# Performance work log

Hardware: AMD Instinct MI355X
Metric: run time of the kernel (lower is better)

The kernel has to match this reference:

```python
import jax, jax.numpy as jnp
import numpy as np

N_NODES = 50000
N_EDGES = 800000
IN_CH = 128
HID_CH = 128


def glorot(key, shape):
    fan_in, fan_out = shape[0], shape[1]
    lim = np.sqrt(6.0 / (fan_in + fan_out)).astype(np.float32)
    return jax.random.uniform(key, shape, jnp.float32, -lim, lim)


def setup_inputs() -> dict:
    key = jax.random.key(0)
    k1, k2, k3, k4 = jax.random.split(key, 4)
    x = jax.random.normal(k1, (N_NODES, IN_CH), jnp.float32)
    edge_index = jax.random.randint(k2, (2, N_EDGES), 0, N_NODES, jnp.int64)
    W1 = glorot(k3, (IN_CH, HID_CH))
    b1 = jnp.zeros((HID_CH,), jnp.float32)
    W2 = glorot(k4, (HID_CH, HID_CH))
    b2 = jnp.zeros((HID_CH,), jnp.float32)
    return {"x": x, "edge_index": edge_index, "W1": W1, "b1": b1, "W2": W2, "b2": b2}


def _gcn_conv(x, W, b, src, dst, n_nodes):
    # PyG GCNConv: h = D^{-1/2} (A + I) D^{-1/2} (x W) + b
    h = x @ W  # [N, H] transform first (as in PyG)
    loops = jnp.arange(n_nodes, dtype=src.dtype)
    s = jnp.concatenate([src, loops])  # add self-loops
    d = jnp.concatenate([dst, loops])
    deg = jnp.zeros((n_nodes,), h.dtype).at[d].add(1.0)
    dinv = jnp.where(deg > 0, jax.lax.rsqrt(deg), 0.0)
    coef = dinv[s] * dinv[d]  # [E+N]
    msg = h[s] * coef[:, None]  # gather + scale
    out = jax.ops.segment_sum(msg, d, num_segments=n_nodes)  # scatter-add
    return out + b


def reference(x, edge_index, W1, b1, W2, b2):
    src, dst = edge_index[0], edge_index[1]
    n = x.shape[0]
    h = jax.nn.relu(_gcn_conv(x, W1, b1, src, dst, n))
    h = jax.nn.relu(_gcn_conv(h, W2, b2, src, dst, n))
    return h
```

## Files before the change

### kernel.cpp

```cpp
#include <hip/hip_runtime.h>

#define N_NODES 50000
#define N_EDGES 800000
#define CH 128
#define NBUCK 196
#define B_BIN 250
#define CHUNK 3200
#define G_GEMM 782

typedef __attribute__((ext_vector_type(8))) short bf16x8;
typedef __attribute__((ext_vector_type(8))) unsigned short u16x8;
typedef __attribute__((ext_vector_type(4))) float f32x4;

__device__ __forceinline__ float bf2f(unsigned short u) {
    union { unsigned int i; float f; } c;
    c.i = ((unsigned int)u) << 16;
    return c.f;
}
__device__ __forceinline__ unsigned short f2bf(float f) {
    union { float f; unsigned int i; } c;
    c.f = f;
    unsigned int lsb = (c.i >> 16) & 1u;
    c.i += 0x7fffu + lsb;
    return (unsigned short)(c.i >> 16);
}

__global__ __launch_bounds__(256) void k_wt(const float* __restrict__ Wa,
                                            const float* __restrict__ Wb,
                                            unsigned short* __restrict__ Wta,
                                            unsigned short* __restrict__ Wtb) {
    const float* W = blockIdx.x ? Wb : Wa;
    unsigned short* Wt = blockIdx.x ? Wtb : Wta;
    const int tid = threadIdx.x;
    for (int i = 0; i < 64; ++i) {
        int idx = i * 256 + tid;
        int n = idx >> 7, kk = idx & 127;
        Wt[idx] = f2bf(W[kk * CH + n]);
    }
}

__global__ __launch_bounds__(256) void k_mega(
        const int* __restrict__ ei, int* __restrict__ blk_base,
        const float* __restrict__ X, const unsigned short* __restrict__ Wt1,
        unsigned short* __restrict__ HS1u) {
    const int tid = threadIdx.x;
    const int b = blockIdx.x;

    if (b < B_BIN) {
        __shared__ int h[NBUCK];
        for (int i = tid; i < NBUCK; i += 256) h[i] = 0;
        __syncthreads();
        const int e0 = b * CHUNK;
        const int* dst = ei + N_EDGES;
        for (int i = tid; i < CHUNK; i += 256)
            atomicAdd(&h[dst[e0 + i] >> 8], 1);
        __syncthreads();
        for (int k = tid; k < NBUCK; k += 256)
            blk_base[b * NBUCK + k] = h[k];
        return;
    }

    const int gb = b - B_BIN;
    const int l = tid & 63, w = tid >> 6;
    const int lm = l & 15, lk = l >> 4;
    const int row0 = gb * 64 + w * 16;

    int arow = row0 + lm;
    if (arow >= N_NODES) arow = N_NODES - 1;
    bf16x8 a[4];
    #pragma unroll
    for (int ki = 0; ki < 4; ++ki) {
        const float* ap = &X[arow * CH + ki * 32 + lk * 8];
        float4 f0 = *(const float4*)ap;
        float4 f1 = *(const float4*)(ap + 4);
        bf16x8 af;
        af[0] = (short)f2bf(f0.x); af[1] = (short)f2bf(f0.y);
        af[2] = (short)f2bf(f0.z); af[3] = (short)f2bf(f0.w);
        af[4] = (short)f2bf(f1.x); af[5] = (short)f2bf(f1.y);
        af[6] = (short)f2bf(f1.z); af[7] = (short)f2bf(f1.w);
        a[ki] = af;
    }

    #pragma unroll
    for (int ct = 0; ct < 8; ++ct) {
        const unsigned short* wp = &Wt1[(ct * 16 + lm) * CH + lk * 8];
        f32x4 acc = {0.f, 0.f, 0.f, 0.f};
        #pragma unroll
        for (int ki = 0; ki < 4; ++ki) {
            bf16x8 bfrag = *(const bf16x8*)&wp[ki * 32];
            acc = __builtin_amdgcn_mfma_f32_16x16x32_bf16(a[ki], bfrag, acc, 0, 0, 0);
        }
        #pragma unroll
        for (int r = 0; r < 4; ++r) {
            int row = row0 + lk * 4 + r;
            if (row < N_NODES)
                HS1u[row * CH + ct * 16 + lm] = f2bf(acc[r]);
        }
    }
}

__global__ __launch_bounds__(256) void k_colscan(int* __restrict__ blk_base,
                                                 int* __restrict__ bucket_cnt) {
    __shared__ int sm[256];
    const int tid = threadIdx.x, k = blockIdx.x;
    int v = (tid < B_BIN) ? blk_base[tid * NBUCK + k] : 0;
    sm[tid] = v;
    __syncthreads();
    #pragma unroll
    for (int off = 1; off < 256; off <<= 1) {
        int t = (tid >= off) ? sm[tid - off] : 0;
        __syncthreads();
        sm[tid] += t;
        __syncthreads();
    }
    if (tid < B_BIN) blk_base[tid * NBUCK + k] = sm[tid] - v;
    if (tid == 255) bucket_cnt[k] = sm[255];
}

__global__ __launch_bounds__(256) void k_bin_place(const int* __restrict__ ei,
                                                   const int* __restrict__ bucket_cnt,
                                                   const int* __restrict__ blk_base,
                                                   unsigned int* __restrict__ ebuf) {
    __shared__ int sm[256];
    __shared__ int bbase[NBUCK];
    __shared__ int h[NBUCK];
    const int tid = threadIdx.x, b = blockIdx.x;

    int v = (tid < NBUCK) ? bucket_cnt[tid] : 0;
    sm[tid] = v;
    __syncthreads();
    #pragma unroll
    for (int off = 1; off < 256; off <<= 1) {
        int t = (tid >= off) ? sm[tid - off] : 0;
        __syncthreads();
        sm[tid] += t;
        __syncthreads();
    }
    if (tid < NBUCK) bbase[tid] = sm[tid] - v;
    for (int i = tid; i < NBUCK; i += 256) h[i] = 0;
    __syncthreads();

    const int e0 = b * CHUNK;
    for (int i = tid; i < CHUNK; i += 256) {
        int s = ei[e0 + i];
        int d = ei[N_EDGES + e0 + i];
        int k = d >> 8;
        int loc = atomicAdd(&h[k], 1);
        int pos = bbase[k] + blk_base[b * NBUCK + k] + loc;
        ebuf[pos] = ((unsigned int)s << 8) | (unsigned int)(d & 255);
    }
}

__global__ __launch_bounds__(256) void k_bucket_cnt(const unsigned int* __restrict__ ebuf,
                                                    const int* __restrict__ bucket_cnt,
                                                    int* __restrict__ rowptr,
                                                    int* __restrict__ degc) {
    __shared__ int cnts[256];
    __shared__ int sm[256];
    __shared__ int e0s;
    const int tid = threadIdx.x, k = blockIdx.x;
    const int node0 = k << 8;

    int vb = (tid < NBUCK) ? bucket_cnt[tid] : 0;
    sm[tid] = vb;
    __syncthreads();
    #pragma unroll
    for (int off = 1; off < 256; off <<= 1) {
        int t = (tid >= off) ? sm[tid - off] : 0;
        __syncthreads();
        sm[tid] += t;
        __syncthreads();
    }
    if (tid == k) e0s = sm[tid] - vb;
    cnts[tid] = 0;
    __syncthreads();
    const int e0 = e0s;
    const int cnt = bucket_cnt[k];

    for (int i = tid; i < cnt; i += 256)
        atomicAdd(&cnts[ebuf[e0 + i] & 255], 1);
    __syncthreads();

    int v = cnts[tid];
    sm[tid] = v;
    __syncthreads();
    #pragma unroll
    for (int off = 1; off < 256; off <<= 1) {
        int t = (tid >= off) ? sm[tid - off] : 0;
        __syncthreads();
        sm[tid] += t;
        __syncthreads();
    }
    int rp = sm[tid] - v;
    int node = node0 + tid;
    if (node < N_NODES) {
        rowptr[node] = e0 + rp;
        int dc = v + 1;
        degc[node] = dc > 255 ? 255 : dc;
    }
    if (k == NBUCK - 1 && tid == 0) rowptr[N_NODES] = N_EDGES;
}

__global__ __launch_bounds__(256) void k_bucket_place(const unsigned int* __restrict__ ebuf,
                                                      const int* __restrict__ rowptr,
                                                      const int* __restrict__ degc,
                                                      int* __restrict__ col) {
    __shared__ int fillc[256];
    const int tid = threadIdx.x, k = blockIdx.x;
    const int node0 = k << 8;

    int node = node0 + tid;
    fillc[tid] = (node < N_NODES) ? rowptr[node] : N_EDGES;
    __syncthreads();
    const int e0 = fillc[0];
    const int e1b = (k == NBUCK - 1) ? N_EDGES : rowptr[node0 + 256];
    const int cnt = e1b - e0;

    for (int i = tid; i < cnt; i += 256) {
        unsigned int pv = ebuf[e0 + i];
        int s = (int)(pv >> 8);
        int j = pv & 255;
        int loc = atomicAdd(&fillc[j], 1);
        col[loc] = (s << 8) | degc[s];
    }
}

template <int MODE>
__global__ __launch_bounds__(256) void k_agg(
        const int* __restrict__ rowptr, const int* __restrict__ col,
        const unsigned short* __restrict__ H,
        const float* __restrict__ b, unsigned short* __restrict__ OUT) {
    int gid = blockIdx.x * 256 + threadIdx.x;
    int node = gid >> 4;
    if (node >= N_NODES) return;
    int lane = gid & 15;
    const u16x8* H8 = (const u16x8*)H;

    int e0 = rowptr[node];
    int e1 = rowptr[node + 1];
    float di = rsqrtf((float)(e1 - e0 + 1));

    u16x8 hv = H8[node * 16 + lane];
    float acc[8];
    #pragma unroll
    for (int j = 0; j < 8; ++j)
        acc[j] = MODE == 0 ? bf2f(hv[j]) * di : bf2f(hv[j]);

    int e = e0;
    for (; e + 3 < e1; e += 4) {
        int c0 = col[e], c1 = col[e + 1], c2 = col[e + 2], c3 = col[e + 3];
        u16x8 v0 = H8[(c0 >> 8) * 16 + lane];
        u16x8 v1 = H8[(c1 >> 8) * 16 + lane];
        u16x8 v2 = H8[(c2 >> 8) * 16 + lane];
        u16x8 v3 = H8[(c3 >> 8) * 16 + lane];
        if (MODE == 0) {
            float d0 = rsqrtf((float)(c0 & 255));
            float d1 = rsqrtf((float)(c1 & 255));
            float d2 = rsqrtf((float)(c2 & 255));
            float d3 = rsqrtf((float)(c3 & 255));
            #pragma unroll
            for (int j = 0; j < 8; ++j)
                acc[j] += (bf2f(v0[j]) * d0 + bf2f(v1[j]) * d1)
                        + (bf2f(v2[j]) * d2 + bf2f(v3[j]) * d3);
        } else {
            #pragma unroll
            for (int j = 0; j < 8; ++j)
                acc[j] += (bf2f(v0[j]) + bf2f(v1[j])) + (bf2f(v2[j]) + bf2f(v3[j]));
        }
    }
    for (; e < e1; ++e) {
        int c0 = col[e];
        u16x8 v = H8[(c0 >> 8) * 16 + lane];
        if (MODE == 0) {
            float ds = rsqrtf((float)(c0 & 255));
            #pragma unroll
            for (int j = 0; j < 8; ++j) acc[j] += bf2f(v[j]) * ds;
        } else {
            #pragma unroll
            for (int j = 0; j < 8; ++j) acc[j] += bf2f(v[j]);
        }
    }

    u16x8 o;
    if (MODE == 0) {
        float4 b0 = *(const float4*)&b[lane * 8];
        float4 b1v = *(const float4*)&b[lane * 8 + 4];
        float bb[8] = {b0.x, b0.y, b0.z, b0.w, b1v.x, b1v.y, b1v.z, b1v.w};
        #pragma unroll
        for (int j = 0; j < 8; ++j)
            o[j] = f2bf(fmaxf(acc[j] * di + bb[j], 0.f) * di);
    } else {
        #pragma unroll
        for (int j = 0; j < 8; ++j)
            o[j] = f2bf(acc[j] * di);
    }
    *(u16x8*)&OUT[node * CH + lane * 8] = o;
}

__global__ __launch_bounds__(256) void k_gemm_out(
        const unsigned short* __restrict__ A2,
        const unsigned short* __restrict__ Wt2,
        const float* __restrict__ b2,
        float* __restrict__ OUT) {
    const int tid = threadIdx.x;
    const int l = tid & 63, w = tid >> 6;
    const int lm = l & 15, lk = l >> 4;
    const int row0 = blockIdx.x * 64 + w * 16;

    int arow = row0 + lm;
    if (arow >= N_NODES) arow = N_NODES - 1;
    bf16x8 a[4];
    #pragma unroll
    for (int ki = 0; ki < 4; ++ki)
        a[ki] = *(const bf16x8*)&A2[arow * CH + ki * 32 + lk * 8];

    #pragma unroll
    for (int ct = 0; ct < 8; ++ct) {
        const unsigned short* wp = &Wt2[(ct * 16 + lm) * CH + lk * 8];
        f32x4 acc = {0.f, 0.f, 0.f, 0.f};
        #pragma unroll
        for (int ki = 0; ki < 4; ++ki) {
            bf16x8 bfrag = *(const bf16x8*)&wp[ki * 32];
            acc = __builtin_amdgcn_mfma_f32_16x16x32_bf16(a[ki], bfrag, acc, 0, 0, 0);
        }
        float bb = b2[ct * 16 + lm];
        #pragma unroll
        for (int r = 0; r < 4; ++r) {
            int row = row0 + lk * 4 + r;
            if (row < N_NODES)
                OUT[row * CH + ct * 16 + lm] = fmaxf(acc[r] + bb, 0.f);
        }
    }
}

extern "C" void kernel_launch(void* const* d_in, const int* in_sizes, int n_in,
                              void* d_out, int out_size, void* d_ws, size_t ws_size,
                              hipStream_t stream) {
    const float* x  = (const float*)d_in[0];
    const int*   ei = (const int*)d_in[1];
    const float* W1 = (const float*)d_in[2];
    const float* b1 = (const float*)d_in[3];
    const float* W2 = (const float*)d_in[4];
    const float* b2 = (const float*)d_in[5];
    float* out = (float*)d_out;

    int* blk_base    = (int*)d_ws;
    int* bucket_cnt  = blk_base + 49152;
    int* rowptr      = bucket_cnt + 256;
    int* degc        = rowptr + 50176;
    int* col         = degc + 50176;
    unsigned int* ebuf = (unsigned int*)(col + 800256);
    unsigned short* hs1u = (unsigned short*)(ebuf + 800256);
    unsigned short* h1p = hs1u + 6400000;
    unsigned short* a2  = h1p + 6400000;
    unsigned short* wt1 = a2 + 6400000;
    unsigned short* wt2 = wt1 + 16384;

    const int gAgg = 3125;

    k_wt<<<2, 256, 0, stream>>>(W1, W2, wt1, wt2);
    k_mega<<<B_BIN + G_GEMM, 256, 0, stream>>>(ei, blk_base, x, wt1, hs1u);
    k_colscan<<<NBUCK, 256, 0, stream>>>(blk_base, bucket_cnt);
    k_bin_place<<<B_BIN, 256, 0, stream>>>(ei, bucket_cnt, blk_base, ebuf);
    k_bucket_cnt<<<NBUCK, 256, 0, stream>>>(ebuf, bucket_cnt, rowptr, degc);
    k_bucket_place<<<NBUCK, 256, 0, stream>>>(ebuf, rowptr, degc, col);
    k_agg<0><<<gAgg, 256, 0, stream>>>(rowptr, col, hs1u, b1, h1p);
    k_agg<1><<<gAgg, 256, 0, stream>>>(rowptr, col, h1p, nullptr, a2);
    k_gemm_out<<<G_GEMM, 256, 0, stream>>>(a2, wt2, b2, out);
}
```

Baseline: 145.2 us.

## Fuse CSR count and place kernels, store degree in separate byte array

Merges the bucket count and bucket placement kernels into a single kernel that computes row pointers and then scatters column indices using shared fill counters. Column entries no longer pack the source degree; instead a compact byte array of clamped degrees is read in the first aggregation pass. This removes a kernel launch and a pass over the edge buffer, at the cost of an extra small dependent gather per edge in the layer-1 aggregation.

```diff
diff --git a/kernel.cpp b/kernel.cpp
--- a/kernel.cpp
+++ b/kernel.cpp
@@ -151,11 +151,13 @@
     }
 }
 
-__global__ __launch_bounds__(256) void k_bucket_cnt(const unsigned int* __restrict__ ebuf,
+__global__ __launch_bounds__(256) void k_bucket_csr(const unsigned int* __restrict__ ebuf,
                                                     const int* __restrict__ bucket_cnt,
                                                     int* __restrict__ rowptr,
-                                                    int* __restrict__ degc) {
+                                                    unsigned char* __restrict__ degc,
+                                                    int* __restrict__ col) {
     __shared__ int cnts[256];
+    __shared__ int fillc[256];
     __shared__ int sm[256];
     __shared__ int e0s;
     const int tid = threadIdx.x, k = blockIdx.x;
@@ -192,42 +194,27 @@
         __syncthreads();
     }
     int rp = sm[tid] - v;
+    fillc[tid] = e0 + rp;
     int node = node0 + tid;
     if (node < N_NODES) {
         rowptr[node] = e0 + rp;
         int dc = v + 1;
-        degc[node] = dc > 255 ? 255 : dc;
+        degc[node] = (unsigned char)(dc > 255 ? 255 : dc);
     }
     if (k == NBUCK - 1 && tid == 0) rowptr[N_NODES] = N_EDGES;
-}
-
-__global__ __launch_bounds__(256) void k_bucket_place(const unsigned int* __restrict__ ebuf,
-                                                      const int* __restrict__ rowptr,
-                                                      const int* __restrict__ degc,
-                                                      int* __restrict__ col) {
-    __shared__ int fillc[256];
-    const int tid = threadIdx.x, k = blockIdx.x;
-    const int node0 = k << 8;
-
-    int node = node0 + tid;
-    fillc[tid] = (node < N_NODES) ? rowptr[node] : N_EDGES;
-    __syncthreads();
-    const int e0 = fillc[0];
-    const int e1b = (k == NBUCK - 1) ? N_EDGES : rowptr[node0 + 256];
-    const int cnt = e1b - e0;
+    __syncthreads();
 
     for (int i = tid; i < cnt; i += 256) {
         unsigned int pv = ebuf[e0 + i];
-        int s = (int)(pv >> 8);
-        int j = pv & 255;
-        int loc = atomicAdd(&fillc[j], 1);
-        col[loc] = (s << 8) | degc[s];
+        int loc = atomicAdd(&fillc[pv & 255], 1);
+        col[loc] = (int)(pv >> 8);
     }
 }
 
 template <int MODE>
 __global__ __launch_bounds__(256) void k_agg(
         const int* __restrict__ rowptr, const int* __restrict__ col,
+        const unsigned char* __restrict__ degc,
         const unsigned short* __restrict__ H,
         const float* __restrict__ b, unsigned short* __restrict__ OUT) {
     int gid = blockIdx.x * 256 + threadIdx.x;
@@ -249,15 +236,15 @@
     int e = e0;
     for (; e + 3 < e1; e += 4) {
         int c0 = col[e], c1 = col[e + 1], c2 = col[e + 2], c3 = col[e + 3];
-        u16x8 v0 = H8[(c0 >> 8) * 16 + lane];
-        u16x8 v1 = H8[(c1 >> 8) * 16 + lane];
-        u16x8 v2 = H8[(c2 >> 8) * 16 + lane];
-        u16x8 v3 = H8[(c3 >> 8) * 16 + lane];
+        u16x8 v0 = H8[c0 * 16 + lane];
+        u16x8 v1 = H8[c1 * 16 + lane];
+        u16x8 v2 = H8[c2 * 16 + lane];
+        u16x8 v3 = H8[c3 * 16 + lane];
         if (MODE == 0) {
-            float d0 = rsqrtf((float)(c0 & 255));
-            float d1 = rsqrtf((float)(c1 & 255));
-            float d2 = rsqrtf((float)(c2 & 255));
-            float d3 = rsqrtf((float)(c3 & 255));
+            float d0 = rsqrtf((float)degc[c0]);
+            float d1 = rsqrtf((float)degc[c1]);
+            float d2 = rsqrtf((float)degc[c2]);
+            float d3 = rsqrtf((float)degc[c3]);
             #pragma unroll
             for (int j = 0; j < 8; ++j)
                 acc[j] += (bf2f(v0[j]) * d0 + bf2f(v1[j]) * d1)
@@ -270,9 +257,9 @@
     }
     for (; e < e1; ++e) {
         int c0 = col[e];
-        u16x8 v = H8[(c0 >> 8) * 16 + lane];
+        u16x8 v = H8[c0 * 16 + lane];
         if (MODE == 0) {
-            float ds = rsqrtf((float)(c0 & 255));
+            float ds = rsqrtf((float)degc[c0]);
             #pragma unroll
             for (int j = 0; j < 8; ++j) acc[j] += bf2f(v[j]) * ds;
         } else {
@@ -347,8 +334,8 @@
     int* blk_base    = (int*)d_ws;
     int* bucket_cnt  = blk_base + 49152;
     int* rowptr      = bucket_cnt + 256;
-    int* degc        = rowptr + 50176;
-    int* col         = degc + 50176;
+    unsigned char* degc = (unsigned char*)(rowptr + 50176);
+    int* col         = rowptr + 50176 + 12544;
     unsigned int* ebuf = (unsigned int*)(col + 800256);
     unsigned short* hs1u = (unsigned short*)(ebuf + 800256);
     unsigned short* h1p = hs1u + 6400000;
@@ -362,9 +349,8 @@
     k_mega<<<B_BIN + G_GEMM, 256, 0, stream>>>(ei, blk_base, x, wt1, hs1u);
     k_colscan<<<NBUCK, 256, 0, stream>>>(blk_base, bucket_cnt);
     k_bin_place<<<B_BIN, 256, 0, stream>>>(ei, bucket_cnt, blk_base, ebuf);
-    k_bucket_cnt<<<NBUCK, 256, 0, stream>>>(ebuf, bucket_cnt, rowptr, degc);
-    k_bucket_place<<<NBUCK, 256, 0, stream>>>(ebuf, rowptr, degc, col);
-    k_agg<0><<<gAgg, 256, 0, stream>>>(rowptr, col, hs1u, b1, h1p);
-    k_agg<1><<<gAgg, 256, 0, stream>>>(rowptr, col, h1p, nullptr, a2);
+    k_bucket_csr<<<NBUCK, 256, 0, stream>>>(ebuf, bucket_cnt, rowptr, degc, col);
+    k_agg<0><<<gAgg, 256, 0, stream>>>(rowptr, col, degc, hs1u, b1, h1p);
+    k_agg<1><<<gAgg, 256, 0, stream>>>(rowptr, col, degc, h1p, nullptr, a2);
     k_gemm_out<<<G_GEMM, 256, 0, stream>>>(a2, wt2, b2, out);
 }
```

After: 142.5 us. No clear change (-1.9%).
